# Optimization experiments

Measured on AMD Instinct MI355X. Metric: run time of the kernel, lower is better.

## Reference

```python
import jax, jax.numpy as jnp
import numpy as np

UNITS = 1024
D_Q = 1024
D_V = 1024


def setup_inputs() -> dict:
    key = jax.random.key(0)
    ks = jax.random.split(key, 8)
    B, S = 32, 2048
    query = jax.random.normal(ks[0], (B, D_Q), dtype=jnp.float32)
    values = jax.random.normal(ks[1], (B, S, D_V), dtype=jnp.float32)
    # Keras Dense params (glorot-ish scale for weights, zero bias init kept random-free)
    W1 = jax.random.normal(ks[2], (D_V, UNITS), dtype=jnp.float32) / np.sqrt(D_V)
    b1 = jnp.zeros((UNITS,), dtype=jnp.float32)
    W2 = jax.random.normal(ks[3], (D_Q, UNITS), dtype=jnp.float32) / np.sqrt(D_Q)
    b2 = jnp.zeros((UNITS,), dtype=jnp.float32)
    V = jax.random.normal(ks[4], (UNITS, 1), dtype=jnp.float32) / np.sqrt(UNITS)
    bV = jnp.zeros((1,), dtype=jnp.float32)
    return {"query": query, "values": values, "W1": W1, "b1": b1,
            "W2": W2, "b2": b2, "V": V, "bV": bV}


def reference(query, values, W1, b1, W2, b2, V, bV):
    # query: [B, d_q], values: [B, S, d_v]
    proj_v = jnp.einsum('bsd,du->bsu', values, W1) + b1        # [B, S, U]
    proj_q = (query @ W2 + b2)[:, None, :]                      # [B, 1, U]
    score = jnp.tanh(proj_v + proj_q) @ V + bV                  # [B, S, 1]
    attention_weights = jax.nn.softmax(score, axis=1)           # [B, S, 1]
    context_vector = jnp.sum(attention_weights * values, axis=1)  # [B, d_v]
    return (context_vector, attention_weights)
```

## Files before the change

kernel.cpp:

```cpp
#include <hip/hip_runtime.h>
#include <math.h>

#define B_  32
#define S_  2048
#define DV  1024
#define U_  1024

typedef __attribute__((ext_vector_type(8))) short bf16x8;
typedef __attribute__((ext_vector_type(4))) float f32x4;

__device__ inline unsigned short f2bf(float f) {
    unsigned int x = __float_as_uint(f);
    return (unsigned short)((x + 0x7fffu + ((x >> 16) & 1u)) >> 16);
}

__device__ inline uint4 pack8(float4 a, float4 b) {
    union { unsigned short s[8]; uint4 u; } p;
    p.s[0] = f2bf(a.x); p.s[1] = f2bf(a.y); p.s[2] = f2bf(a.z); p.s[3] = f2bf(a.w);
    p.s[4] = f2bf(b.x); p.s[5] = f2bf(b.y); p.s[6] = f2bf(b.z); p.s[7] = f2bf(b.w);
    return p.u;
}

__device__ inline float tanh_fast(float x) {
    float ax = fabsf(x);
    float e  = __expf(ax + ax);
    float t  = 1.0f - __fdividef(2.0f, e + 1.0f);
    return copysignf(t, x);
}

__device__ __forceinline__ void gload16(const void* g, void* l) {
    __builtin_amdgcn_global_load_lds(
        (const __attribute__((address_space(1))) void*)g,
        (__attribute__((address_space(3))) void*)l,
        16, 0, 0);
}

#define ASM_VMCNT(N) asm volatile("s_waitcnt vmcnt(" #N ")" ::: "memory")
#define ASM_LGKM0()  do { asm volatile("s_waitcnt lgkmcnt(0)" ::: "memory"); \
                          __builtin_amdgcn_sched_barrier(0); } while (0)

__global__ __launch_bounds__(256)
void prep_small(const float* __restrict__ W1, unsigned short* __restrict__ W1T,
                const float* __restrict__ query, const float* __restrict__ W2,
                const float* __restrict__ b1, const float* __restrict__ b2,
                float* __restrict__ t, float* __restrict__ scores,
                float* __restrict__ ctx) {
    const int bid = blockIdx.x;
    const int tid = threadIdx.x;

    if (bid < 256) {
        __shared__ float tile[64][65];
        int k0 = (bid & 15) * 64, u0 = (bid >> 4) * 64;
        int lr = tid >> 4, lc = (tid & 15) * 4;
#pragma unroll
        for (int j = 0; j < 4; ++j) {
            float4 f = *(const float4*)&W1[(size_t)(k0 + lr + j * 16) * U_ + u0 + lc];
            tile[lr + j * 16][lc + 0] = f.x; tile[lr + j * 16][lc + 1] = f.y;
            tile[lr + j * 16][lc + 2] = f.z; tile[lr + j * 16][lc + 3] = f.w;
        }
        __syncthreads();
        int ur = tid >> 2, kq = (tid & 3) * 16;
        union { unsigned short s[8]; uint4 u; } p0, p1;
#pragma unroll
        for (int e = 0; e < 8; ++e) p0.s[e] = f2bf(tile[kq + e][ur]);
#pragma unroll
        for (int e = 0; e < 8; ++e) p1.s[e] = f2bf(tile[kq + 8 + e][ur]);
        unsigned short* dst = W1T + (size_t)(u0 + ur) * 1024 + k0 + kq;
        *(uint4*)dst       = p0.u;
        *(uint4*)(dst + 8) = p1.u;
    } else if (bid < 384) {
        __shared__ float qs2[1024];
        int i = bid - 256;
        int b = i >> 2, uq = i & 3;
        for (int j = tid; j < 1024; j += 256) qs2[j] = query[b * DV + j];
        __syncthreads();
        int u = uq * 256 + tid;
        float a0 = 0.f, a1 = 0.f, a2 = 0.f, a3 = 0.f;
        float a4 = 0.f, a5 = 0.f, a6 = 0.f, a7 = 0.f;
        const float* w = W2 + u;
        for (int k = 0; k < 1024; k += 8) {
            a0 += qs2[k + 0] * w[(size_t)(k + 0) * U_];
            a1 += qs2[k + 1] * w[(size_t)(k + 1) * U_];
            a2 += qs2[k + 2] * w[(size_t)(k + 2) * U_];
            a3 += qs2[k + 3] * w[(size_t)(k + 3) * U_];
            a4 += qs2[k + 4] * w[(size_t)(k + 4) * U_];
            a5 += qs2[k + 5] * w[(size_t)(k + 5) * U_];
            a6 += qs2[k + 6] * w[(size_t)(k + 6) * U_];
            a7 += qs2[k + 7] * w[(size_t)(k + 7) * U_];
        }
        t[b * U_ + u] = b1[u] + b2[u]
                      + ((a0 + a1) + (a2 + a3)) + ((a4 + a5) + (a6 + a7));
    } else if (bid < 640) {
        scores[(bid - 384) * 256 + tid] = 0.f;
    } else {
        ctx[(bid - 640) * 256 + tid] = 0.f;
    }
}

#define MFMA16(MB, NB)                                                          \
    _Pragma("unroll") for (int ks = 0; ks < 2; ++ks)                            \
    _Pragma("unroll") for (int n = 0; n < 2; ++n)                               \
    _Pragma("unroll") for (int m = 0; m < 4; ++m)                               \
        acc[(MB)+m][(NB)+n] = __builtin_amdgcn_mfma_f32_16x16x32_bf16(          \
            af[m][ks], bf[n][ks], acc[(MB)+m][(NB)+n], 0, 0, 0);

#define ISSUEA(Sa, Sb, Sc, Sd, kt, h) do {                                      \
    const float4* _s = (const float4*)(aRow + (size_t)(h) * 131072 + (kt) * 64);\
    Sa = _s[0]; Sb = _s[1]; Sc = _s[2]; Sd = _s[3]; } while (0)

#define WRITEA(Sa, Sb, Sc, Sd, dOff) do {                                       \
    *(uint4*)(lds + (dOff) + wO0) = pack8(Sa, Sb);                              \
    *(uint4*)(lds + (dOff) + wO1) = pack8(Sc, Sd); } while (0)

__launch_bounds__(512, 2)
__global__ void scores_mfma8f(const float* __restrict__ values,
                              const unsigned short* __restrict__ W1T,
                              const float* __restrict__ tvec,
                              const float* __restrict__ V,
                              float* __restrict__ scores) {
    __shared__ __align__(16) char lds[131072];

    const int tid  = threadIdx.x;
    const int lane = tid & 63;
    const int wave = tid >> 6;
    const int wm   = wave >> 2;
    const int wn   = wave & 3;
    const int l15  = lane & 15;
    const int lq   = lane >> 4;

    const int id    = blockIdx.x;
    const int wg    = (id & 7) * 128 + (id >> 3);
    const int utile = wg & 3;
    const int stile = wg >> 2;
    const size_t row0 = (size_t)stile * 256;
    const int b       = (int)(row0 >> 11);
    const int s_local = (int)(row0 & 2047);
    const int u0      = utile * 256;

    const int rowst = wave * 8 + (lane >> 3);
    const int kch8  = ((lane & 7) ^ ((lane >> 3) & 7)) * 8;
    const unsigned short* bSrc = W1T + (size_t)(u0 + rowst) * 1024 + kch8;
    char* const dstW = lds + wave * 1024;

    const int rA  = tid >> 2;
    const int kcA = tid & 3;
    const int c0  = (2 * kcA) ^ (rA & 7);
    const int wO0 = rA * 128 + c0 * 16;
    const int wO1 = rA * 128 + (c0 ^ 1) * 16;
    const float* aRow = values + (row0 + rA) * 1024 + kcA * 16;

    const int ao0 = wm * 16384 + l15 * 128 + ((lq ^ (l15 & 7)) << 4);
    const int ao1 = ao0 ^ 64;
    const int bo0 = 32768 + (wn >> 1) * 16384 + (wn & 1) * 8192
                  + l15 * 128 + ((lq ^ (l15 & 7)) << 4);
    const int bo1 = bo0 ^ 64;

    f32x4 acc[8][4];
#pragma unroll
    for (int m = 0; m < 8; ++m)
#pragma unroll
        for (int n = 0; n < 4; ++n) acc[m][n] = (f32x4)0.f;

    bf16x8 af[4][2];
    bf16x8 bf[2][2];

    auto stageB = [&](const unsigned short* s, int dOff) {
        gload16(s,             dstW + dOff);
        gload16(s + 64 * 1024, dstW + dOff + 8192);
    };
    auto readA4 = [&](int base) {
#pragma unroll
        for (int m = 0; m < 4; ++m) {
            af[m][0] = *(const bf16x8*)(lds + base + m * 2048 + ao0);
            af[m][1] = *(const bf16x8*)(lds + base + m * 2048 + ao1);
        }
    };
    auto readB2 = [&](int base) {
#pragma unroll
        for (int n = 0; n < 2; ++n) {
            bf[n][0] = *(const bf16x8*)(lds + base + n * 2048 + bo0);
            bf[n][1] = *(const bf16x8*)(lds + base + n * 2048 + bo1);
        }
    };

    float4 s0a, s0b, s0c, s0d;
    float4 s1a, s1b, s1c, s1d;
    float4 s2a, s2b, s2c, s2d;

    ISSUEA(s0a, s0b, s0c, s0d, 0, 0);
    ISSUEA(s2a, s2b, s2c, s2d, 0, 1);
    stageB(bSrc,          32768);
    stageB(bSrc + 131072, 49152);
    ISSUEA(s1a, s1b, s1c, s1d, 1, 0);
    ASM_VMCNT(8);
    WRITEA(s0a, s0b, s0c, s0d, 0);
    WRITEA(s2a, s2b, s2c, s2d, 16384);
    ASM_VMCNT(4);
    ASM_LGKM0();
    __builtin_amdgcn_s_barrier();
    __builtin_amdgcn_sched_barrier(0);

    for (int it = 0; it < 8; ++it) {
        const bool pf = (it < 7);
        ISSUEA(s0a, s0b, s0c, s0d, 2 * it + 1, 1);
        ASM_VMCNT(4);
        WRITEA(s1a, s1b, s1c, s1d, 65536);
        readA4(0);
        readB2(0);
        __builtin_amdgcn_s_barrier();
        ASM_LGKM0();
        __builtin_amdgcn_s_setprio(1);
        MFMA16(0, 0);
        __builtin_amdgcn_s_setprio(0);
        __builtin_amdgcn_s_barrier();
        stageB(bSrc + 64, 98304);
        ASM_VMCNT(2);
        WRITEA(s0a, s0b, s0c, s0d, 81920);
        readB2(2 * 2048);
        __builtin_amdgcn_s_barrier();
        ASM_LGKM0();
        __builtin_amdgcn_s_setprio(1);
        MFMA16(0, 2);
        __builtin_amdgcn_s_setprio(0);
        __builtin_amdgcn_s_barrier();
        stageB(bSrc + 64 + 131072, 114688);
        readA4(4 * 2048);
        __builtin_amdgcn_s_barrier();
        ASM_LGKM0();
        __builtin_amdgcn_s_setprio(1);
        MFMA16(4, 2);
        __builtin_amdgcn_s_setprio(0);
        __builtin_amdgcn_s_barrier();
        readB2(0);
        if (pf) ISSUEA(s1a, s1b, s1c, s1d, 2 * it + 2, 0);
        __builtin_amdgcn_s_barrier();
        ASM_LGKM0();
        __builtin_amdgcn_s_setprio(1);
        MFMA16(4, 0);
        __builtin_amdgcn_s_setprio(0);
        __builtin_amdgcn_sched_barrier(0);
        if (pf) { ASM_VMCNT(4); } else { ASM_VMCNT(0); }
        __builtin_amdgcn_s_barrier();
        __builtin_amdgcn_sched_barrier(0);
        if (pf) {
            ISSUEA(s0a, s0b, s0c, s0d, 2 * it + 2, 1);
            ASM_VMCNT(4);
            WRITEA(s1a, s1b, s1c, s1d, 0);
        }
        readA4(65536);
        readB2(65536);
        __builtin_amdgcn_s_barrier();
        ASM_LGKM0();
        __builtin_amdgcn_s_setprio(1);
        MFMA16(0, 0);
        __builtin_amdgcn_s_setprio(0);
        __builtin_amdgcn_s_barrier();
        readB2(65536 + 2 * 2048);
        if (pf) {
            stageB(bSrc + 128, 32768);
            ASM_VMCNT(2);
            WRITEA(s0a, s0b, s0c, s0d, 16384);
        }
        __builtin_amdgcn_s_barrier();
        ASM_LGKM0();
        __builtin_amdgcn_s_setprio(1);
        MFMA16(0, 2);
        __builtin_amdgcn_s_setprio(0);
        __builtin_amdgcn_s_barrier();
        if (pf) stageB(bSrc + 128 + 131072, 49152);
        readA4(65536 + 4 * 2048);
        __builtin_amdgcn_s_barrier();
        ASM_LGKM0();
        __builtin_amdgcn_s_setprio(1);
        MFMA16(4, 2);
        __builtin_amdgcn_s_setprio(0);
        __builtin_amdgcn_s_barrier();
        readB2(65536);
        if (pf) ISSUEA(s1a, s1b, s1c, s1d, 2 * it + 3, 0);
        __builtin_amdgcn_s_barrier();
        ASM_LGKM0();
        __builtin_amdgcn_s_setprio(1);
        MFMA16(4, 0);
        __builtin_amdgcn_s_setprio(0);
        __builtin_amdgcn_sched_barrier(0);
        if (pf) { ASM_VMCNT(4); }
        __builtin_amdgcn_s_barrier();
        __builtin_amdgcn_sched_barrier(0);

        bSrc += 128;
    }

    __syncthreads();
    float* fscore = (float*)lds;
    if (tid < 256) fscore[tid] = 0.f;
    __syncthreads();
    float tu[4], vu[4];
#pragma unroll
    for (int n = 0; n < 4; ++n) {
        int u = u0 + wn * 64 + n * 16 + l15;
        tu[n] = tvec[b * U_ + u];
        vu[n] = V[u];
    }
#pragma unroll
    for (int m = 0; m < 8; ++m) {
#pragma unroll
        for (int r = 0; r < 4; ++r) {
            float p = 0.f;
#pragma unroll
            for (int n = 0; n < 4; ++n) p += tanh_fast(acc[m][n][r] + tu[n]) * vu[n];
            p += __shfl_xor(p, 1);
            p += __shfl_xor(p, 2);
            p += __shfl_xor(p, 4);
            p += __shfl_xor(p, 8);
            if (l15 == 0) atomicAdd(&fscore[wm * 128 + m * 16 + lq * 4 + r], p);
        }
    }
    __syncthreads();
    if (tid < 256) atomicAdd(&scores[(size_t)b * S_ + s_local + tid], fscore[tid]);
}

__global__ __launch_bounds__(256)
void fused_sm_ctx(const float* __restrict__ scores, const float* __restrict__ values,
                  float* __restrict__ wout, float* __restrict__ ctx) {
    const int b   = blockIdx.x;
    const int sc  = blockIdx.y;
    const int tid = threadIdx.x;
    __shared__ float red[256];
    __shared__ float ws_[128];

    float v[8];
    float m = -1e30f;
#pragma unroll
    for (int i = 0; i < 8; ++i) {
        v[i] = scores[(size_t)b * S_ + tid + i * 256];
        m = fmaxf(m, v[i]);
    }
    red[tid] = m; __syncthreads();
    for (int off = 128; off > 0; off >>= 1) {
        if (tid < off) red[tid] = fmaxf(red[tid], red[tid + off]);
        __syncthreads();
    }
    m = red[0];
    __syncthreads();
    float s = 0.f;
#pragma unroll
    for (int i = 0; i < 8; ++i) s += __expf(v[i] - m);
    red[tid] = s; __syncthreads();
    for (int off = 128; off > 0; off >>= 1) {
        if (tid < off) red[tid] += red[tid + off];
        __syncthreads();
    }
    float inv = 1.f / red[0];
    __syncthreads();

    if (tid < 128) {
        float x = scores[(size_t)b * S_ + sc * 128 + tid];
        float w = __expf(x - m) * inv;
        ws_[tid] = w;
        wout[(size_t)b * S_ + sc * 128 + tid] = w;
    }
    __syncthreads();

    const float4* vp = (const float4*)(values + ((size_t)b * S_ + sc * 128) * DV) + tid;
    float ax = 0.f, ay = 0.f, az = 0.f, aw = 0.f;
#pragma unroll 4
    for (int s2 = 0; s2 < 128; ++s2) {
        float4 vv = vp[(size_t)s2 * 256];
        float wv = ws_[s2];
        ax += wv * vv.x; ay += wv * vv.y; az += wv * vv.z; aw += wv * vv.w;
    }
    float* c = ctx + b * DV + tid * 4;
    atomicAdd(c + 0, ax); atomicAdd(c + 1, ay);
    atomicAdd(c + 2, az); atomicAdd(c + 3, aw);
}

__global__ void init_kernel(const float* __restrict__ b1, const float* __restrict__ b2,
                            float* __restrict__ t, float* __restrict__ ctx,
                            float* __restrict__ scores) {
    int i = blockIdx.x * 256 + threadIdx.x;
    scores[i] = 0.f;
    if (i < B_ * U_) {
        int u = i & (U_ - 1);
        t[i]   = b1[u] + b2[u];
        ctx[i] = 0.f;
    }
}

__global__ void projq_kernel(const float* __restrict__ q, const float* __restrict__ W2,
                             float* __restrict__ t) {
    int b  = blockIdx.x;
    int ks = blockIdx.y;
    int tid = threadIdx.x;
    __shared__ float qs[64];
    if (tid < 64) qs[tid] = q[b * DV + ks * 64 + tid];
    __syncthreads();
    float a0 = 0.f, a1 = 0.f, a2 = 0.f, a3 = 0.f;
    const float* w = W2 + (size_t)(ks * 64) * U_;
    for (int d = 0; d < 64; ++d) {
        float qd = qs[d];
        const float* wr = w + (size_t)d * U_ + tid;
        a0 += qd * wr[0];
        a1 += qd * wr[256];
        a2 += qd * wr[512];
        a3 += qd * wr[768];
    }
    atomicAdd(&t[b * U_ + tid      ], a0);
    atomicAdd(&t[b * U_ + tid + 256], a1);
    atomicAdd(&t[b * U_ + tid + 512], a2);
    atomicAdd(&t[b * U_ + tid + 768], a3);
}

__launch_bounds__(256, 2)
__global__ void scores_vec(const float* __restrict__ values, const float* __restrict__ W1,
                           const float* __restrict__ t, const float* __restrict__ V,
                           float* __restrict__ scores) {
    __shared__ float vA[16][132];
    __shared__ float vB[16][68];
    __shared__ float fscore[128];
    const int b   = blockIdx.y;
    const int s0  = blockIdx.x * 128;
    const int tid = threadIdx.x;
    const int tx  = tid & 15, ty = tid >> 4;
    if (tid < 128) fscore[tid] = 0.f;
    const float* vbase = values + ((size_t)b * S_ + s0) * (size_t)DV;
    const int lm = tid >> 2, lkq = (tid & 3) * 4;
    const int lbk = tid >> 4, lbj = (tid & 15) * 4;
    for (int nt = 0; nt < U_ / 64; ++nt) {
        const int u0 = nt * 64;
        float acc[8][4];
#pragma unroll
        for (int i = 0; i < 8; ++i)
#pragma unroll
            for (int j = 0; j < 4; ++j) acc[i][j] = 0.f;
        for (int k0 = 0; k0 < DV; k0 += 16) {
            __syncthreads();
            const float4 v0 = *(const float4*)(vbase + (size_t)lm * DV + k0 + lkq);
            const float4 v1 = *(const float4*)(vbase + (size_t)(lm + 64) * DV + k0 + lkq);
            vA[lkq + 0][lm] = v0.x; vA[lkq + 1][lm] = v0.y;
            vA[lkq + 2][lm] = v0.z; vA[lkq + 3][lm] = v0.w;
            vA[lkq + 0][lm + 64] = v1.x; vA[lkq + 1][lm + 64] = v1.y;
            vA[lkq + 2][lm + 64] = v1.z; vA[lkq + 3][lm + 64] = v1.w;
            *(float4*)&vB[lbk][lbj] = *(const float4*)(W1 + (size_t)(k0 + lbk) * U_ + u0 + lbj);
            __syncthreads();
#pragma unroll
            for (int k = 0; k < 16; ++k) {
                float4 va0 = *(const float4*)&vA[k][ty * 8];
                float4 va1 = *(const float4*)&vA[k][ty * 8 + 4];
                float4 vb  = *(const float4*)&vB[k][tx * 4];
                float a_[8] = {va0.x, va0.y, va0.z, va0.w, va1.x, va1.y, va1.z, va1.w};
                float b_[4] = {vb.x, vb.y, vb.z, vb.w};
#pragma unroll
                for (int i = 0; i < 8; ++i)
#pragma unroll
                    for (int j = 0; j < 4; ++j) acc[i][j] += a_[i] * b_[j];
            }
        }
        float tq[4], vv[4];
#pragma unroll
        for (int j = 0; j < 4; ++j) {
            int u = u0 + tx * 4 + j;
            tq[j] = t[b * U_ + u];
            vv[j] = V[u];
        }
#pragma unroll
        for (int i = 0; i < 8; ++i) {
            float p = 0.f;
#pragma unroll
            for (int j = 0; j < 4; ++j) p += tanhf(acc[i][j] + tq[j]) * vv[j];
            p += __shfl_down(p, 8, 16);
            p += __shfl_down(p, 4, 16);
            p += __shfl_down(p, 2, 16);
            p += __shfl_down(p, 1, 16);
            if (tx == 0) fscore[ty * 8 + i] += p;
        }
    }
    __syncthreads();
    if (tid < 128) scores[(size_t)b * S_ + s0 + tid] = fscore[tid];
}

__global__ void softmax_kernel(const float* __restrict__ scores, float* __restrict__ wout) {
    int b = blockIdx.x;
    int tid = threadIdx.x;
    __shared__ float red[256];
    float v[8];
    float m = -1e30f;
#pragma unroll
    for (int i = 0; i < 8; ++i) {
        v[i] = scores[(size_t)b * S_ + tid + i * 256];
        m = fmaxf(m, v[i]);
    }
    red[tid] = m; __syncthreads();
    for (int off = 128; off > 0; off >>= 1) {
        if (tid < off) red[tid] = fmaxf(red[tid], red[tid + off]);
        __syncthreads();
    }
    m = red[0];
    __syncthreads();
    float s = 0.f;
#pragma unroll
    for (int i = 0; i < 8; ++i) { v[i] = __expf(v[i] - m); s += v[i]; }
    red[tid] = s; __syncthreads();
    for (int off = 128; off > 0; off >>= 1) {
        if (tid < off) red[tid] += red[tid + off];
        __syncthreads();
    }
    float inv = 1.f / red[0];
#pragma unroll
    for (int i = 0; i < 8; ++i) wout[(size_t)b * S_ + tid + i * 256] = v[i] * inv;
}

__global__ void context_kernel(const float* __restrict__ values, const float* __restrict__ w,
                               float* __restrict__ ctx) {
    int b   = blockIdx.x;
    int sc  = blockIdx.y;
    int tid = threadIdx.x;
    __shared__ float ws_[128];
    if (tid < 128) ws_[tid] = w[(size_t)b * S_ + sc * 128 + tid];
    __syncthreads();
    const float4* vp = (const float4*)(values + ((size_t)b * S_ + sc * 128) * DV) + tid;
    float ax = 0.f, ay = 0.f, az = 0.f, aw = 0.f;
#pragma unroll 4
    for (int s = 0; s < 128; ++s) {
        float4 v = vp[(size_t)s * 256];
        float wv = ws_[s];
        ax += wv * v.x; ay += wv * v.y; az += wv * v.z; aw += wv * v.w;
    }
    float* c = ctx + b * DV + tid * 4;
    atomicAdd(c + 0, ax); atomicAdd(c + 1, ay);
    atomicAdd(c + 2, az); atomicAdd(c + 3, aw);
}

extern "C" void kernel_launch(void* const* d_in, const int* in_sizes, int n_in,
                              void* d_out, int out_size, void* d_ws, size_t ws_size,
                              hipStream_t stream) {
    const float* query  = (const float*)d_in[0];
    const float* values = (const float*)d_in[1];
    const float* W1     = (const float*)d_in[2];
    const float* b1     = (const float*)d_in[3];
    const float* W2     = (const float*)d_in[4];
    const float* b2     = (const float*)d_in[5];
    const float* V      = (const float*)d_in[6];

    float* out  = (float*)d_out;
    float* ctx  = out;
    float* wout = out + B_ * DV;

    char* ws = (char*)d_ws;
    const size_t W1T_BYTES = (size_t)U_ * DV * 2;
    const size_t T_BYTES   = (size_t)B_ * U_ * 4;
    const size_t SC_BYTES  = (size_t)B_ * S_ * 4;

    if (ws_size >= W1T_BYTES + T_BYTES + SC_BYTES) {
        unsigned short* W1T = (unsigned short*)ws;
        float* t      = (float*)(ws + W1T_BYTES);
        float* scores = t + B_ * U_;

        prep_small   <<<dim3(768),    256, 0, stream>>>(W1, W1T, query, W2,
                                                        b1, b2, t, scores, ctx);
        scores_mfma8f<<<dim3(1024),   512, 0, stream>>>(values, W1T, t, V, scores);
        fused_sm_ctx <<<dim3(32, 16), 256, 0, stream>>>(scores, values, wout, ctx);
    } else {
        float* t      = (float*)ws;
        float* scores = t + B_ * U_;

        init_kernel   <<<dim3(256),      256, 0, stream>>>(b1, b2, t, ctx, scores);
        projq_kernel  <<<dim3(32, 16),   256, 0, stream>>>(query, W2, t);
        scores_vec    <<<dim3(16, 32),   256, 0, stream>>>(values, W1, t, V, scores);
        softmax_kernel<<<dim3(32),       256, 0, stream>>>(scores, wout);
        context_kernel<<<dim3(32, 16),   256, 0, stream>>>(values, wout, ctx);
    }
}
```

Before: 660.9 us.

## Pre-convert values to swizzled bf16 tiles and stage A via direct LDS loads

Adds a separate kernel that converts the fp32 values tensor into a pre-swizzled bf16 tiled layout in workspace. The scores GEMM can then stage A with global_load_lds directly, with no register round-trip or in-loop packing. The context atomics are replaced by per-chunk partial sums plus a small reduction kernel. The cost is an extra full pass over values (256MB read, 128MB written) and a larger workspace, in exchange for a leaner, better-pipelined GEMM main loop.

After: 674.6 us. +2.1%, slower.

```diff
diff --git a/kernel.cpp b/kernel.cpp
--- a/kernel.cpp
+++ b/kernel.cpp
@@ -43,8 +43,7 @@
 void prep_small(const float* __restrict__ W1, unsigned short* __restrict__ W1T,
                 const float* __restrict__ query, const float* __restrict__ W2,
                 const float* __restrict__ b1, const float* __restrict__ b2,
-                float* __restrict__ t, float* __restrict__ scores,
-                float* __restrict__ ctx) {
+                float* __restrict__ t, float* __restrict__ scores) {
     const int bid = blockIdx.x;
     const int tid = threadIdx.x;
 
@@ -90,10 +89,30 @@
         }
         t[b * U_ + u] = b1[u] + b2[u]
                       + ((a0 + a1) + (a2 + a3)) + ((a4 + a5) + (a6 + a7));
-    } else if (bid < 640) {
+    } else {
         scores[(bid - 384) * 256 + tid] = 0.f;
-    } else {
-        ctx[(bid - 640) * 256 + tid] = 0.f;
+    }
+}
+
+__global__ __launch_bounds__(256)
+void cvt_lines(const float* __restrict__ v, char* __restrict__ o) {
+    const int bid   = blockIdx.x;
+    const int stile = bid >> 4;
+    const int kt    = bid & 15;
+    const int tid   = threadIdx.x;
+    const int h     = tid >> 7;
+    const int r     = tid & 127;
+    const int row   = stile * 256 + h * 128 + r;
+    const float4* src = (const float4*)(v + (size_t)row * 1024 + kt * 64);
+    float4 f[16];
+#pragma unroll
+    for (int j = 0; j < 16; ++j) f[j] = src[j];
+    char* dst = o + (size_t)stile * 524288 + kt * 32768 + h * 16384 + r * 128;
+    const int rx = r & 7;
+#pragma unroll
+    for (int c = 0; c < 8; ++c) {
+        uint4 w = pack8(f[2 * c], f[2 * c + 1]);
+        *(uint4*)(dst + ((c ^ rx) << 4)) = w;
     }
 }
 
@@ -104,20 +123,12 @@
         acc[(MB)+m][(NB)+n] = __builtin_amdgcn_mfma_f32_16x16x32_bf16(          \
             af[m][ks], bf[n][ks], acc[(MB)+m][(NB)+n], 0, 0, 0);
 
-#define ISSUEA(Sa, Sb, Sc, Sd, kt, h) do {                                      \
-    const float4* _s = (const float4*)(aRow + (size_t)(h) * 131072 + (kt) * 64);\
-    Sa = _s[0]; Sb = _s[1]; Sc = _s[2]; Sd = _s[3]; } while (0)
-
-#define WRITEA(Sa, Sb, Sc, Sd, dOff) do {                                       \
-    *(uint4*)(lds + (dOff) + wO0) = pack8(Sa, Sb);                              \
-    *(uint4*)(lds + (dOff) + wO1) = pack8(Sc, Sd); } while (0)
-
 __launch_bounds__(512, 2)
-__global__ void scores_mfma8f(const float* __restrict__ values,
-                              const unsigned short* __restrict__ W1T,
-                              const float* __restrict__ tvec,
-                              const float* __restrict__ V,
-                              float* __restrict__ scores) {
+__global__ void scores_mfma8(const char* __restrict__ AbfT,
+                             const unsigned short* __restrict__ W1T,
+                             const float* __restrict__ tvec,
+                             const float* __restrict__ V,
+                             float* __restrict__ scores) {
     __shared__ __align__(16) char lds[131072];
 
     const int tid  = threadIdx.x;
@@ -137,17 +148,11 @@
     const int s_local = (int)(row0 & 2047);
     const int u0      = utile * 256;
 
+    const char* aBase = AbfT + (size_t)stile * 524288 + wave * 1024 + lane * 16;
     const int rowst = wave * 8 + (lane >> 3);
     const int kch8  = ((lane & 7) ^ ((lane >> 3) & 7)) * 8;
     const unsigned short* bSrc = W1T + (size_t)(u0 + rowst) * 1024 + kch8;
     char* const dstW = lds + wave * 1024;
-
-    const int rA  = tid >> 2;
-    const int kcA = tid & 3;
-    const int c0  = (2 * kcA) ^ (rA & 7);
-    const int wO0 = rA * 128 + c0 * 16;
-    const int wO1 = rA * 128 + (c0 ^ 1) * 16;
-    const float* aRow = values + (row0 + rA) * 1024 + kcA * 16;
 
     const int ao0 = wm * 16384 + l15 * 128 + ((lq ^ (l15 & 7)) << 4);
     const int ao1 = ao0 ^ 64;
@@ -164,6 +169,10 @@
     bf16x8 af[4][2];
     bf16x8 bf[2][2];
 
+    auto stageA = [&](size_t gOff, int dOff) {
+        gload16(aBase + gOff,        dstW + dOff);
+        gload16(aBase + gOff + 8192, dstW + dOff + 8192);
+    };
     auto stageB = [&](const unsigned short* s, int dOff) {
         gload16(s,             dstW + dOff);
         gload16(s + 64 * 1024, dstW + dOff + 8192);
@@ -183,48 +192,38 @@
         }
     };
 
-    float4 s0a, s0b, s0c, s0d;
-    float4 s1a, s1b, s1c, s1d;
-    float4 s2a, s2b, s2c, s2d;
-
-    ISSUEA(s0a, s0b, s0c, s0d, 0, 0);
-    ISSUEA(s2a, s2b, s2c, s2d, 0, 1);
+    stageA(0,     0);
+    stageA(16384, 16384);
     stageB(bSrc,          32768);
     stageB(bSrc + 131072, 49152);
-    ISSUEA(s1a, s1b, s1c, s1d, 1, 0);
-    ASM_VMCNT(8);
-    WRITEA(s0a, s0b, s0c, s0d, 0);
-    WRITEA(s2a, s2b, s2c, s2d, 16384);
-    ASM_VMCNT(4);
-    ASM_LGKM0();
+    stageA(32768, 65536);
+    __builtin_amdgcn_sched_barrier(0);
+    ASM_VMCNT(2);
     __builtin_amdgcn_s_barrier();
     __builtin_amdgcn_sched_barrier(0);
 
     for (int it = 0; it < 8; ++it) {
         const bool pf = (it < 7);
-        ISSUEA(s0a, s0b, s0c, s0d, 2 * it + 1, 1);
-        ASM_VMCNT(4);
-        WRITEA(s1a, s1b, s1c, s1d, 65536);
+        const size_t aIt = (size_t)it * 65536;
         readA4(0);
         readB2(0);
+        stageA(aIt + 49152, 81920);
         __builtin_amdgcn_s_barrier();
         ASM_LGKM0();
         __builtin_amdgcn_s_setprio(1);
         MFMA16(0, 0);
         __builtin_amdgcn_s_setprio(0);
         __builtin_amdgcn_s_barrier();
+        readB2(2 * 2048);
         stageB(bSrc + 64, 98304);
-        ASM_VMCNT(2);
-        WRITEA(s0a, s0b, s0c, s0d, 81920);
-        readB2(2 * 2048);
         __builtin_amdgcn_s_barrier();
         ASM_LGKM0();
         __builtin_amdgcn_s_setprio(1);
         MFMA16(0, 2);
         __builtin_amdgcn_s_setprio(0);
         __builtin_amdgcn_s_barrier();
+        readA4(4 * 2048);
         stageB(bSrc + 64 + 131072, 114688);
-        readA4(4 * 2048);
         __builtin_amdgcn_s_barrier();
         ASM_LGKM0();
         __builtin_amdgcn_s_setprio(1);
@@ -232,23 +231,19 @@
         __builtin_amdgcn_s_setprio(0);
         __builtin_amdgcn_s_barrier();
         readB2(0);
-        if (pf) ISSUEA(s1a, s1b, s1c, s1d, 2 * it + 2, 0);
+        if (pf) stageA(aIt + 65536, 0);
         __builtin_amdgcn_s_barrier();
         ASM_LGKM0();
         __builtin_amdgcn_s_setprio(1);
         MFMA16(4, 0);
         __builtin_amdgcn_s_setprio(0);
         __builtin_amdgcn_sched_barrier(0);
-        if (pf) { ASM_VMCNT(4); } else { ASM_VMCNT(0); }
+        if (pf) { ASM_VMCNT(2); } else { ASM_VMCNT(0); }
         __builtin_amdgcn_s_barrier();
         __builtin_amdgcn_sched_barrier(0);
-        if (pf) {
-            ISSUEA(s0a, s0b, s0c, s0d, 2 * it + 2, 1);
-            ASM_VMCNT(4);
-            WRITEA(s1a, s1b, s1c, s1d, 0);
-        }
         readA4(65536);
         readB2(65536);
+        if (pf) stageA(aIt + 81920, 16384);
         __builtin_amdgcn_s_barrier();
         ASM_LGKM0();
         __builtin_amdgcn_s_setprio(1);
@@ -256,11 +251,7 @@
         __builtin_amdgcn_s_setprio(0);
         __builtin_amdgcn_s_barrier();
         readB2(65536 + 2 * 2048);
-        if (pf) {
-            stageB(bSrc + 128, 32768);
-            ASM_VMCNT(2);
-            WRITEA(s0a, s0b, s0c, s0d, 16384);
-        }
+        if (pf) stageB(bSrc + 128, 32768);
         __builtin_amdgcn_s_barrier();
         ASM_LGKM0();
         __builtin_amdgcn_s_setprio(1);
@@ -276,14 +267,14 @@
         __builtin_amdgcn_s_setprio(0);
         __builtin_amdgcn_s_barrier();
         readB2(65536);
-        if (pf) ISSUEA(s1a, s1b, s1c, s1d, 2 * it + 3, 0);
+        if (pf) stageA(aIt + 98304, 65536);
         __builtin_amdgcn_s_barrier();
         ASM_LGKM0();
         __builtin_amdgcn_s_setprio(1);
         MFMA16(4, 0);
         __builtin_amdgcn_s_setprio(0);
         __builtin_amdgcn_sched_barrier(0);
-        if (pf) { ASM_VMCNT(4); }
+        if (pf) { ASM_VMCNT(2); }
         __builtin_amdgcn_s_barrier();
         __builtin_amdgcn_sched_barrier(0);
 
@@ -320,8 +311,8 @@
 }
 
 __global__ __launch_bounds__(256)
-void fused_sm_ctx(const float* __restrict__ scores, const float* __restrict__ values,
-                  float* __restrict__ wout, float* __restrict__ ctx) {
+void sm_ctx_part(const float* __restrict__ scores, const float* __restrict__ values,
+                 float* __restrict__ wout, float* __restrict__ ctxp) {
     const int b   = blockIdx.x;
     const int sc  = blockIdx.y;
     const int tid = threadIdx.x;
@@ -369,9 +360,20 @@
         float wv = ws_[s2];
         ax += wv * vv.x; ay += wv * vv.y; az += wv * vv.z; aw += wv * vv.w;
     }
-    float* c = ctx + b * DV + tid * 4;
-    atomicAdd(c + 0, ax); atomicAdd(c + 1, ay);
-    atomicAdd(c + 2, az); atomicAdd(c + 3, aw);
+    float4 outv; outv.x = ax; outv.y = ay; outv.z = az; outv.w = aw;
+    *(float4*)(ctxp + ((size_t)(b * 16 + sc)) * 1024 + tid * 4) = outv;
+}
+
+__global__ __launch_bounds__(256)
+void ctx_reduce(const float* __restrict__ ctxp, float* __restrict__ ctx) {
+    const int b  = blockIdx.x;
+    const int dq = blockIdx.y;
+    const int d  = dq * 256 + threadIdx.x;
+    const float* p = ctxp + (size_t)b * 16 * 1024 + d;
+    float s = 0.f;
+#pragma unroll
+    for (int sc = 0; sc < 16; ++sc) s += p[sc * 1024];
+    ctx[b * DV + d] = s;
 }
 
 __global__ void init_kernel(const float* __restrict__ b1, const float* __restrict__ b2,
@@ -546,19 +548,25 @@
     float* wout = out + B_ * DV;
 
     char* ws = (char*)d_ws;
-    const size_t W1T_BYTES = (size_t)U_ * DV * 2;
-    const size_t T_BYTES   = (size_t)B_ * U_ * 4;
-    const size_t SC_BYTES  = (size_t)B_ * S_ * 4;
-
-    if (ws_size >= W1T_BYTES + T_BYTES + SC_BYTES) {
+    const size_t W1T_BYTES  = (size_t)U_ * DV * 2;
+    const size_t T_BYTES    = (size_t)B_ * U_ * 4;
+    const size_t SC_BYTES   = (size_t)B_ * S_ * 4;
+    const size_t CTXP_BYTES = (size_t)B_ * 16 * DV * 4;
+    const size_t ABF_BYTES  = (size_t)B_ * S_ * DV * 2;
+
+    if (ws_size >= W1T_BYTES + T_BYTES + SC_BYTES + CTXP_BYTES + ABF_BYTES) {
         unsigned short* W1T = (unsigned short*)ws;
         float* t      = (float*)(ws + W1T_BYTES);
         float* scores = t + B_ * U_;
-
-        prep_small   <<<dim3(768),    256, 0, stream>>>(W1, W1T, query, W2,
-                                                        b1, b2, t, scores, ctx);
-        scores_mfma8f<<<dim3(1024),   512, 0, stream>>>(values, W1T, t, V, scores);
-        fused_sm_ctx <<<dim3(32, 16), 256, 0, stream>>>(scores, values, wout, ctx);
+        float* ctxp   = scores + B_ * S_;
+        char*  AbfT   = (char*)(ctxp + B_ * 16 * DV);
+
+        prep_small  <<<dim3(640),    256, 0, stream>>>(W1, W1T, query, W2,
+                                                       b1, b2, t, scores);
+        cvt_lines   <<<dim3(4096),   256, 0, stream>>>(values, AbfT);
+        scores_mfma8<<<dim3(1024),   512, 0, stream>>>(AbfT, W1T, t, V, scores);
+        sm_ctx_part <<<dim3(32, 16), 256, 0, stream>>>(scores, values, wout, ctxp);
+        ctx_reduce  <<<dim3(32, 4),  256, 0, stream>>>(ctxp, ctx);
     } else {
         float* t      = (float*)ws;
         float* scores = t + B_ * U_;
```
